# Performance work log

Measured on AMD Instinct MI355X. Metric: run time of the kernel, lower is better.

The kernel has to match this reference:

```python
import jax, jax.numpy as jnp
import numpy as np
from jax import lax

K = 8          # num_classes
C_IN = 256     # in_channels
EPS = 1e-5


def resize_bilinear_ac(x, H, W):
    """Bilinear resize with align_corners=True. x: [B,C,h,w] -> [B,C,H,W]."""
    B, C, h, w = x.shape
    if h == H and w == W:
        return x
    ys = jnp.linspace(0.0, h - 1.0, H)
    xs = jnp.linspace(0.0, w - 1.0, W)
    y0 = jnp.floor(ys).astype(jnp.int32)
    x0 = jnp.floor(xs).astype(jnp.int32)
    y1 = jnp.minimum(y0 + 1, h - 1)
    x1 = jnp.minimum(x0 + 1, w - 1)
    wy = (ys - y0.astype(x.dtype))[None, None, :, None]
    wx = (xs - x0.astype(x.dtype))[None, None, None, :]
    g00 = x[:, :, y0][:, :, :, x0]
    g01 = x[:, :, y0][:, :, :, x1]
    g10 = x[:, :, y1][:, :, :, x0]
    g11 = x[:, :, y1][:, :, :, x1]
    top = g00 * (1.0 - wx) + g01 * wx
    bot = g10 * (1.0 - wx) + g11 * wx
    return top * (1.0 - wy) + bot * wy


def setup_inputs() -> dict:
    key = jax.random.key(0)
    ks = jax.random.split(key, 16)
    shapes = [(2, 256, 128, 128), (2, 256, 64, 64), (2, 256, 32, 32), (2, 256, 16, 16), (2, 256, 8, 8)]
    inp = {}
    for i, s in enumerate(shapes):
        inp[f"feat{i}"] = jax.random.normal(ks[i], s, dtype=jnp.float32)
    inp["attr_feat"] = jax.random.normal(ks[5], (2, K * C_IN, 64, 64), dtype=jnp.float32)
    # learned params
    inp["mlp_f_w"] = jax.random.normal(ks[6], (256, 256), dtype=jnp.float32) * 0.02
    inp["mlp_f_b"] = jnp.zeros((256,), dtype=jnp.float32)
    inp["mlp_a_w"] = jax.random.normal(ks[7], (256, 256), dtype=jnp.float32) * 0.02
    inp["mlp_a_b"] = jnp.zeros((256,), dtype=jnp.float32)
    # 5 grouped convs: [out=2048, in_per_group=256, 3, 3] each, no bias (BN follows)
    inp["conv_w"] = jax.random.normal(ks[8], (5, K * C_IN, C_IN, 3, 3), dtype=jnp.float32) * 0.02
    inp["bn_gamma"] = jnp.ones((5, K * C_IN), dtype=jnp.float32)
    inp["bn_beta"] = jnp.zeros((5, K * C_IN), dtype=jnp.float32)
    inp["bn_mean"] = jax.random.normal(ks[9], (5, K * C_IN), dtype=jnp.float32) * 0.1
    inp["bn_var"] = jax.random.uniform(ks[10], (5, K * C_IN), dtype=jnp.float32, minval=0.5, maxval=1.5)
    return inp


def _forward(feats, attr_feat, mlp_f_w, mlp_f_b, mlp_a_w, mlp_a_b, conv_w, bn_gamma, bn_beta, bn_mean, bn_var):
    B = attr_feat.shape[0]
    # global avg pool attr -> [B, K, C] -> mlp_a
    avg_attr = attr_feat.mean(axis=(2, 3)).reshape(B, K, C_IN)
    avg_attr = avg_attr @ mlp_a_w.T + mlp_a_b  # [B,K,256]
    outs = []
    for i, x in enumerate(feats):
        _, C, H, W = x.shape
        avg_x = x.mean(axis=(2, 3)) @ mlp_f_w.T + mlp_f_b          # [B,256]
        logits = jnp.einsum('bkc,bc->bk', avg_attr, avg_x)          # [B,K]
        attn = jax.nn.softmax(logits, axis=-1)
        y = resize_bilinear_ac(attr_feat, H, W)                      # [B,2048,H,W]
        y = lax.conv_general_dilated(
            y, conv_w[i], window_strides=(1, 1), padding=((1, 1), (1, 1)),
            dimension_numbers=('NCHW', 'OIHW', 'NCHW'), feature_group_count=K)
        inv = lax.rsqrt(bn_var[i] + EPS)
        y = (y - bn_mean[i][None, :, None, None]) * (inv * bn_gamma[i])[None, :, None, None] + bn_beta[i][None, :, None, None]
        y = jax.nn.relu(y)
        y = y.reshape(B, K, C, H, W)
        y = jnp.einsum('bkchw,bk->bchw', y, attn)                   # weighted sum over classes
        outs.append(jax.nn.relu(x + y))
    return tuple(outs)


def reference(feat0, feat1, feat2, feat3, feat4, attr_feat, mlp_f_w, mlp_f_b, mlp_a_w, mlp_a_b, conv_w, bn_gamma, bn_beta, bn_mean, bn_var):
    feats = [feat0, feat1, feat2, feat3, feat4]
    return _forward(feats, attr_feat, mlp_f_w, mlp_f_b, mlp_a_w, mlp_a_b, conv_w, bn_gamma, bn_beta, bn_mean, bn_var)
```

## Files before the change

kernel.cpp:

```cpp
#include <hip/hip_runtime.h>
#include <hip/hip_bf16.h>
#include <cstdint>

typedef __attribute__((ext_vector_type(8))) short short8;
typedef __attribute__((ext_vector_type(4))) float f32x4;

#define EPSV 1e-5f

__device__ __forceinline__ void gload_lds16(const void* g, void* l) {
  __builtin_amdgcn_global_load_lds(
      (const __attribute__((address_space(1))) void*)(uintptr_t)g,
      (__attribute__((address_space(3))) void*)(uint32_t)(uintptr_t)l,
      16, 0, 0);
}

__global__ void mean_kernel(const float* __restrict__ in, float* __restrict__ out,
                            int HW, float inv) {
  const int ch = blockIdx.x;
  const int t = threadIdx.x;
  const float* p = in + (size_t)ch * HW;
  float s = 0.f;
  const int nv = HW >> 2;
  const float4* pv = (const float4*)p;
  for (int i = t; i < nv; i += 256) { float4 v = pv[i]; s += v.x + v.y + v.z + v.w; }
  __shared__ float red[256];
  red[t] = s; __syncthreads();
  for (int off = 128; off > 0; off >>= 1) {
    if (t < off) red[t] += red[t + off];
    __syncthreads();
  }
  if (t == 0) out[ch] = red[0] * inv;
}

__global__ void wtrans_kernel(const float* __restrict__ cw,
                              const float* __restrict__ gamma, const float* __restrict__ beta,
                              const float* __restrict__ mean, const float* __restrict__ var,
                              __hip_bfloat16* __restrict__ wt, float* __restrict__ bias) {
  const int oc = blockIdx.x;
  const int i  = blockIdx.y;
  const int ci = threadIdx.x;
  const int idx = i * 2048 + oc;
  const float sc = rsqrtf(var[idx] + EPSV) * gamma[idx];
  if (ci == 0) bias[idx] = beta[idx] - mean[idx] * sc;
  const int g = oc >> 8, co = oc & 255;
  const float* src = cw + ((size_t)idx * 256 + ci) * 9;
  const size_t dbase = (size_t)(i * 8 + g) * 9 * 65536 + co * 256 + ci;
#pragma unroll
  for (int tap = 0; tap < 9; ++tap)
    wt[dbase + (size_t)tap * 65536] = __float2bfloat16(src[tap] * sc);
}

__global__ void gate_kernel(const float* __restrict__ meanA, const float* __restrict__ meanF,
                            const float* __restrict__ Wa, const float* __restrict__ ba,
                            const float* __restrict__ Wf, const float* __restrict__ bfp,
                            float* __restrict__ attn) {
  __shared__ float mA[16 * 256];
  __shared__ float mF[10 * 256];
  __shared__ float pA[16 * 256];
  __shared__ float pF[10 * 256];
  __shared__ float lg[80];
  const int t = threadIdx.x;
  for (int i = t; i < 4096; i += 256) mA[i] = meanA[i];
  for (int i = t; i < 2560; i += 256) mF[i] = meanF[i];
  __syncthreads();
  {
    float acc[16];
#pragma unroll
    for (int j = 0; j < 16; ++j) acc[j] = 0.f;
    for (int ci = 0; ci < 256; ++ci) {
      const float w = Wa[t * 256 + ci];
#pragma unroll
      for (int j = 0; j < 16; ++j) acc[j] += mA[j * 256 + ci] * w;
    }
    const float bb = ba[t];
#pragma unroll
    for (int j = 0; j < 16; ++j) pA[j * 256 + t] = acc[j] + bb;
  }
  {
    float acc[10];
#pragma unroll
    for (int j = 0; j < 10; ++j) acc[j] = 0.f;
    for (int ci = 0; ci < 256; ++ci) {
      const float w = Wf[t * 256 + ci];
#pragma unroll
      for (int j = 0; j < 10; ++j) acc[j] += mF[j * 256 + ci] * w;
    }
    const float bb = bfp[t];
#pragma unroll
    for (int j = 0; j < 10; ++j) pF[j * 256 + t] = acc[j] + bb;
  }
  __syncthreads();
  if (t < 80) {
    const int i = t >> 4, r = t & 15, b = r >> 3, k = r & 7;
    const float* a = &pA[(b * 8 + k) * 256];
    const float* f = &pF[(i * 2 + b) * 256];
    float d = 0.f;
    for (int c = 0; c < 256; ++c) d += a[c] * f[c];
    lg[t] = d;
  }
  __syncthreads();
  if (t < 10) {
    const int base = t * 8;
    float m = lg[base];
    for (int k = 1; k < 8; ++k) m = fmaxf(m, lg[base + k]);
    float e[8], s = 0.f;
    for (int k = 0; k < 8; ++k) { e[k] = __expf(lg[base + k] - m); s += e[k]; }
    const float invs = 1.f / s;
    for (int k = 0; k < 8; ++k) attn[base + k] = e[k] * invs;
  }
}

__global__ void resize_kernel(const float* __restrict__ attr,
                              __hip_bfloat16* __restrict__ R,
                              int W, int Hp, int Wp, float scl) {
  const int bk = blockIdx.x;
  const int yp = blockIdx.y;
  const int t  = threadIdx.x;
  const size_t rowbase = ((size_t)bk * Hp + yp) * (size_t)Wp * 256;
  if (yp == 0 || yp == Hp - 1) {
    uint32_t* p = (uint32_t*)(R + rowbase);
    const int n = Wp * 128;
    for (int idx = t; idx < n; idx += 256) p[idx] = 0u;
    return;
  }
  const int y = yp - 1;
  const float fy = y * scl;
  int y0 = (int)floorf(fy); if (y0 > 63) y0 = 63;
  const float wy = fy - (float)y0;
  const int y1 = min(y0 + 1, 63);
  __shared__ float buf[2][64][65];
  const int cc = t >> 2, seg = (t & 3) * 16;
  const int bb = bk >> 3, k = bk & 7;
  const float* ab = attr + (size_t)bb * 2048 * 4096;
  const int ci = t & 63;
  for (int cq = 0; cq < 4; ++cq) {
    __syncthreads();
    {
      const int ch = k * 256 + cq * 64 + cc;
      const float* r0 = ab + ((size_t)ch * 64 + y0) * 64;
      const float* r1 = ab + ((size_t)ch * 64 + y1) * 64;
#pragma unroll
      for (int u = 0; u < 4; ++u) {
        float4 v0 = ((const float4*)r0)[(t & 3) * 4 + u];
        float4 v1 = ((const float4*)r1)[(t & 3) * 4 + u];
        buf[0][cc][seg + u * 4 + 0] = v0.x; buf[0][cc][seg + u * 4 + 1] = v0.y;
        buf[0][cc][seg + u * 4 + 2] = v0.z; buf[0][cc][seg + u * 4 + 3] = v0.w;
        buf[1][cc][seg + u * 4 + 0] = v1.x; buf[1][cc][seg + u * 4 + 1] = v1.y;
        buf[1][cc][seg + u * 4 + 2] = v1.z; buf[1][cc][seg + u * 4 + 3] = v1.w;
      }
    }
    __syncthreads();
    for (int x = t >> 6; x < W; x += 4) {
      const float fx = x * scl;
      int x0 = (int)floorf(fx); if (x0 > 63) x0 = 63;
      const float wx = fx - (float)x0;
      const int x1 = min(x0 + 1, 63);
      const float top = buf[0][ci][x0] * (1.f - wx) + buf[0][ci][x1] * wx;
      const float bot = buf[1][ci][x0] * (1.f - wx) + buf[1][ci][x1] * wx;
      R[rowbase + (size_t)(x + 1) * 256 + cq * 64 + ci] = __float2bfloat16(top * (1.f - wy) + bot * wy);
    }
    if (t < 64) {
      R[rowbase + cq * 64 + t] = __float2bfloat16(0.f);
      R[rowbase + (size_t)(Wp - 1) * 256 + cq * 64 + t] = __float2bfloat16(0.f);
    }
  }
}

__device__ __forceinline__ void issue_stage(
    const __hip_bfloat16* __restrict__ Wt, const __hip_bfloat16* __restrict__ Rb,
    size_t rgstride, int gp, int typ, int txp, int cqp, int Wp,
    const int* aoff, const int* adst, const int* boff, const int* bdst,
    __hip_bfloat16* bufA, __hip_bfloat16* bufB) {
  const __hip_bfloat16* wp = Wt + (((size_t)gp * 9 + typ * 3 + txp) << 16) + (cqp << 6);
  const __hip_bfloat16* rp = Rb + (size_t)gp * rgstride + ((typ * Wp + txp) << 8) + (cqp << 6);
#pragma unroll
  for (int q = 0; q < 4; ++q) gload_lds16(wp + aoff[q], bufA + adst[q]);
#pragma unroll
  for (int q = 0; q < 2; ++q) gload_lds16(rp + boff[q], bufB + bdst[q]);
}

__global__ __launch_bounds__(512, 2)
void conv_kernel(const __hip_bfloat16* __restrict__ R,
                 const __hip_bfloat16* __restrict__ Wt,
                 const float* __restrict__ bias,
                 const float* __restrict__ attn,
                 const float* __restrict__ featp,
                 float* __restrict__ outp,
                 int W, int lw, int Hp, int Wp, int HW,
                 int b0, int NB, int gcount) {
  __shared__ alignas(16) __hip_bfloat16 ldsA[3][256 * 64];
  __shared__ alignas(16) __hip_bfloat16 ldsB[3][128 * 64];
  const int tid  = threadIdx.x;
  const int lane = tid & 63;
  const int wave = __builtin_amdgcn_readfirstlane(tid >> 6);
  const int wm = (wave >> 1) * 64;
  const int wn = (wave & 1) * 64;
  const int n0  = blockIdx.x * 128;
  const int bb  = (int)blockIdx.y % NB;
  const int gs  = (int)blockIdx.y / NB;
  const int b   = b0 + bb;
  const int g0  = gs * gcount;

  const int c8 = lane & 7;
  const int r8 = lane >> 3;
  int aoff[4], adst[4], boff[2], bdst[2];
#pragma unroll
  for (int q = 0; q < 4; ++q) {
    const int row = wave * 32 + q * 8 + r8;
    aoff[q] = (row << 8) + ((c8 ^ (row & 7)) << 3);
    adst[q] = (wave * 32 + q * 8) << 6;
  }
#pragma unroll
  for (int q = 0; q < 2; ++q) {
    const int row = wave * 16 + q * 8 + r8;
    int sg = n0 + row; if (sg >= HW) sg = HW - 1;
    const int y = sg >> lw, x = sg & (W - 1);
    boff[q] = ((y * Wp + x) << 8) + ((c8 ^ (row & 7)) << 3);
    bdst[q] = (wave * 16 + q * 8) << 6;
  }

  const size_t rgstride = (size_t)Hp * Wp * 256;
  const __hip_bfloat16* Rb = R + (size_t)bb * 8 * rgstride;

  const f32x4 fz = {0.f, 0.f, 0.f, 0.f};
  f32x4 fin[4][4], acc[4][4];
#pragma unroll
  for (int mf = 0; mf < 4; ++mf)
#pragma unroll
    for (int nf = 0; nf < 4; ++nf) { fin[mf][nf] = fz; acc[mf][nf] = fz; }

  issue_stage(Wt, Rb, rgstride, g0, 0, 0, 0, Wp, aoff, adst, boff, bdst,
              &ldsA[0][0], &ldsB[0][0]);
  issue_stage(Wt, Rb, rgstride, g0, 0, 0, 1, Wp, aoff, adst, boff, bdst,
              &ldsA[1][0], &ldsB[1][0]);
  int cqp = 1, txp = 0, typ = 0, gp = g0;
  int cur = 0, nbf = 2;
  int foldc = 0, gcur = g0;
  const int nstages = gcount * 36;

  for (int s = 0; s < nstages; ++s) {
    __builtin_amdgcn_s_barrier();
    asm volatile("" ::: "memory");
    if (s + 2 < nstages) {
      ++cqp;
      if (cqp == 4) {
        cqp = 0; ++txp;
        if (txp == 3) { txp = 0; ++typ; if (typ == 3) { typ = 0; ++gp; } }
      }
      issue_stage(Wt, Rb, rgstride, gp, typ, txp, cqp, Wp, aoff, adst, boff, bdst,
                  &ldsA[nbf][0], &ldsB[nbf][0]);
      asm volatile("s_waitcnt vmcnt(12)" ::: "memory");
    } else if (s + 1 < nstages) {
      asm volatile("s_waitcnt vmcnt(6)" ::: "memory");
    } else {
      asm volatile("s_waitcnt vmcnt(0)" ::: "memory");
    }
    __builtin_amdgcn_s_barrier();
    asm volatile("" ::: "memory");

    const __hip_bfloat16* pA = &ldsA[cur][0];
    const __hip_bfloat16* pB = &ldsB[cur][0];
#pragma unroll
    for (int ks = 0; ks < 2; ++ks) {
      short8 af[4], bfv[4];
      const int cb = ks * 4 + (lane >> 4);
#pragma unroll
      for (int mf = 0; mf < 4; ++mf) {
        const int row = wm + mf * 16 + (lane & 15);
        af[mf] = *(const short8*)&pA[(row << 6) + ((cb ^ (row & 7)) << 3)];
      }
#pragma unroll
      for (int nf = 0; nf < 4; ++nf) {
        const int row = wn + nf * 16 + (lane & 15);
        bfv[nf] = *(const short8*)&pB[(row << 6) + ((cb ^ (row & 7)) << 3)];
      }
#pragma unroll
      for (int mf = 0; mf < 4; ++mf)
#pragma unroll
        for (int nf = 0; nf < 4; ++nf)
          acc[mf][nf] = __builtin_amdgcn_mfma_f32_16x16x32_bf16(
              af[mf], bfv[nf], acc[mf][nf], 0, 0, 0);
    }

    if (++cur == 3) cur = 0;
    if (++nbf == 3) nbf = 0;

    if (++foldc == 36) {
      foldc = 0;
      const float aw = attn[b * 8 + gcur];
#pragma unroll
      for (int mf = 0; mf < 4; ++mf) {
        const int cobase = wm + mf * 16 + ((lane >> 4) << 2);
#pragma unroll
        for (int r = 0; r < 4; ++r) {
          const float bs = bias[(gcur << 8) + cobase + r];
#pragma unroll
          for (int nf = 0; nf < 4; ++nf) {
            fin[mf][nf][r] += aw * fmaxf(acc[mf][nf][r] + bs, 0.f);
            acc[mf][nf][r] = 0.f;
          }
        }
      }
      ++gcur;
    }
  }

  const size_t plane = (size_t)256 * HW;
  if (featp) {
    const float* fb = featp + (size_t)b * plane;
    float* ob = outp + (size_t)b * plane;
#pragma unroll
    for (int mf = 0; mf < 4; ++mf) {
      const int cobase = wm + mf * 16 + ((lane >> 4) << 2);
#pragma unroll
      for (int nf = 0; nf < 4; ++nf) {
        const int n = n0 + wn + nf * 16 + (lane & 15);
        if (n < HW) {
#pragma unroll
          for (int r = 0; r < 4; ++r) {
            const size_t idx = (size_t)(cobase + r) * HW + n;
            ob[idx] = fmaxf(fb[idx] + fin[mf][nf][r], 0.f);
          }
        }
      }
    }
  } else {
    float* zb = outp + ((size_t)gs * 2 + b) * plane;
#pragma unroll
    for (int mf = 0; mf < 4; ++mf) {
      const int cobase = wm + mf * 16 + ((lane >> 4) << 2);
#pragma unroll
      for (int nf = 0; nf < 4; ++nf) {
        const int n = n0 + wn + nf * 16 + (lane & 15);
        if (n < HW) {
#pragma unroll
          for (int r = 0; r < 4; ++r)
            zb[(size_t)(cobase + r) * HW + n] = fin[mf][nf][r];
        }
      }
    }
  }
}

__global__ void reduce_kernel(const float* __restrict__ z, const float* __restrict__ feat,
                              float* __restrict__ outp, int total, int S) {
  const int idx = blockIdx.x * 256 + threadIdx.x;
  if (idx >= total) return;
  float s = feat[idx];
  for (int j = 0; j < S; ++j) s += z[(size_t)j * total + idx];
  outp[idx] = fmaxf(s, 0.f);
}

extern "C" void kernel_launch(void* const* d_in, const int* in_sizes, int n_in,
                              void* d_out, int out_size, void* d_ws, size_t ws_size,
                              hipStream_t stream) {
  const float* feat[5];
  for (int i = 0; i < 5; ++i) feat[i] = (const float*)d_in[i];
  const float* attr = (const float*)d_in[5];
  const float* mfw = (const float*)d_in[6];
  const float* mfb = (const float*)d_in[7];
  const float* maw = (const float*)d_in[8];
  const float* mab = (const float*)d_in[9];
  const float* cw  = (const float*)d_in[10];
  const float* bng = (const float*)d_in[11];
  const float* bnb = (const float*)d_in[12];
  const float* bnm = (const float*)d_in[13];
  const float* bnv = (const float*)d_in[14];
  float* out = (float*)d_out;

  char* ws = (char*)d_ws;
  float* attnW = (float*)(ws);
  float* meanA = (float*)(ws + 512);
  float* meanF = (float*)(ws + 20480);
  float* biasW = (float*)(ws + 32768);
  __hip_bfloat16* Wt = (__hip_bfloat16*)(ws + 131072);
  const size_t R_OFF = 47316992;
  __hip_bfloat16* Rbuf = (__hip_bfloat16*)(ws + R_OFF);

  const bool full = ws_size >= (size_t)219316224;
  const int NB = full ? 2 : 1;
  float* zbuf = (float*)(ws + R_OFF + (size_t)NB * 69222400);

  static const int HS[5] = {128, 64, 32, 16, 8};
  static const size_t OOFF[5] = {0, 8388608, 10485760, 11010048, 11141120};
  static const int SPLIT[5] = {1, 4, 8, 8, 8};

  mean_kernel<<<4096, 256, 0, stream>>>(attr, meanA, 4096, 1.f / 4096.f);
  for (int i = 0; i < 5; ++i) {
    const int HW = HS[i] * HS[i];
    mean_kernel<<<512, 256, 0, stream>>>(feat[i], meanF + i * 512, HW, 1.f / (float)HW);
  }
  wtrans_kernel<<<dim3(2048, 5), 256, 0, stream>>>(cw, bng, bnb, bnm, bnv, Wt, biasW);
  gate_kernel<<<1, 256, 0, stream>>>(meanA, meanF, maw, mab, mfw, mfb, attnW);

  for (int i = 0; i < 5; ++i) {
    const int H = HS[i], W = H, HW = H * W, Hp = H + 2, Wp = W + 2;
    const int lw = 31 - __builtin_clz((unsigned)W);
    const float scl = 63.f / (float)(H - 1);
    const int S = full ? SPLIT[i] : 1;
    const int gcount = 8 / S;
    for (int b0 = 0; b0 < 2; b0 += NB) {
      resize_kernel<<<dim3(NB * 8, Hp), 256, 0, stream>>>(
          attr + (size_t)b0 * 2048 * 4096, Rbuf, W, Hp, Wp, scl);
      const float* fp = (S == 1) ? feat[i] : nullptr;
      float* op = (S == 1) ? (out + OOFF[i]) : zbuf;
      conv_kernel<<<dim3((HW + 127) / 128, NB * S), 512, 0, stream>>>(
          Rbuf, Wt + (size_t)i * 8 * 9 * 65536, biasW + i * 2048, attnW + i * 16,
          fp, op, W, lw, Hp, Wp, HW, b0, NB, gcount);
    }
    if (S > 1) {
      const int total = 2 * 256 * HW;
      reduce_kernel<<<(total + 255) / 256, 256, 0, stream>>>(zbuf, feat[i], out + OOFF[i], total, S);
    }
  }
}
```

Baseline: 822.7 us.

## Split main loop into ping-pong LDS-read/MFMA phases with barriers and setprio

Restructures the GEMM main loop so each stage is two half-K phases. Each phase reads fragments from LDS, issues the next global-to-LDS prefetch, then runs its MFMA cluster at raised wave priority between barriers. The vmcnt waits are moved and the prologue now waits before the loop starts. The aim is to interleave waves so LDS reads and global loads overlap other waves' MFMA work. The cost is more barriers per stage and a tighter, easy-to-get-wrong wait/hazard ordering across the triple-buffered LDS.

```diff
diff --git a/kernel.cpp b/kernel.cpp
--- a/kernel.cpp
+++ b/kernel.cpp
@@ -233,14 +233,33 @@
               &ldsA[0][0], &ldsB[0][0]);
   issue_stage(Wt, Rb, rgstride, g0, 0, 0, 1, Wp, aoff, adst, boff, bdst,
               &ldsA[1][0], &ldsB[1][0]);
+  asm volatile("s_waitcnt vmcnt(6)" ::: "memory");
+  __builtin_amdgcn_s_barrier();
+  asm volatile("" ::: "memory");
+
   int cqp = 1, txp = 0, typ = 0, gp = g0;
   int cur = 0, nbf = 2;
   int foldc = 0, gcur = g0;
   const int nstages = gcount * 36;
 
   for (int s = 0; s < nstages; ++s) {
-    __builtin_amdgcn_s_barrier();
-    asm volatile("" ::: "memory");
+    const __hip_bfloat16* pA = &ldsA[cur][0];
+    const __hip_bfloat16* pB = &ldsB[cur][0];
+    short8 af[4], bfv[4];
+
+    {
+      const int cb = lane >> 4;
+#pragma unroll
+      for (int mf = 0; mf < 4; ++mf) {
+        const int row = wm + mf * 16 + (lane & 15);
+        af[mf] = *(const short8*)&pA[(row << 6) + ((cb ^ (row & 7)) << 3)];
+      }
+#pragma unroll
+      for (int nf = 0; nf < 4; ++nf) {
+        const int row = wn + nf * 16 + (lane & 15);
+        bfv[nf] = *(const short8*)&pB[(row << 6) + ((cb ^ (row & 7)) << 3)];
+      }
+    }
     if (s + 2 < nstages) {
       ++cqp;
       if (cqp == 4) {
@@ -249,21 +268,22 @@
       }
       issue_stage(Wt, Rb, rgstride, gp, typ, txp, cqp, Wp, aoff, adst, boff, bdst,
                   &ldsA[nbf][0], &ldsB[nbf][0]);
-      asm volatile("s_waitcnt vmcnt(12)" ::: "memory");
-    } else if (s + 1 < nstages) {
-      asm volatile("s_waitcnt vmcnt(6)" ::: "memory");
-    } else {
-      asm volatile("s_waitcnt vmcnt(0)" ::: "memory");
-    }
+    }
+    __builtin_amdgcn_s_barrier();
+    __builtin_amdgcn_sched_barrier(0);
+    __builtin_amdgcn_s_setprio(1);
+#pragma unroll
+    for (int mf = 0; mf < 4; ++mf)
+#pragma unroll
+      for (int nf = 0; nf < 4; ++nf)
+        acc[mf][nf] = __builtin_amdgcn_mfma_f32_16x16x32_bf16(
+            af[mf], bfv[nf], acc[mf][nf], 0, 0, 0);
+    __builtin_amdgcn_s_setprio(0);
     __builtin_amdgcn_s_barrier();
     asm volatile("" ::: "memory");
 
-    const __hip_bfloat16* pA = &ldsA[cur][0];
-    const __hip_bfloat16* pB = &ldsB[cur][0];
-#pragma unroll
-    for (int ks = 0; ks < 2; ++ks) {
-      short8 af[4], bfv[4];
-      const int cb = ks * 4 + (lane >> 4);
+    {
+      const int cb = 4 + (lane >> 4);
 #pragma unroll
       for (int mf = 0; mf < 4; ++mf) {
         const int row = wm + mf * 16 + (lane & 15);
@@ -274,13 +294,21 @@
         const int row = wn + nf * 16 + (lane & 15);
         bfv[nf] = *(const short8*)&pB[(row << 6) + ((cb ^ (row & 7)) << 3)];
       }
-#pragma unroll
-      for (int mf = 0; mf < 4; ++mf)
-#pragma unroll
-        for (int nf = 0; nf < 4; ++nf)
-          acc[mf][nf] = __builtin_amdgcn_mfma_f32_16x16x32_bf16(
-              af[mf], bfv[nf], acc[mf][nf], 0, 0, 0);
-    }
+    }
+    if (s + 2 < nstages)      asm volatile("s_waitcnt vmcnt(6)" ::: "memory");
+    else if (s + 1 < nstages) asm volatile("s_waitcnt vmcnt(0)" ::: "memory");
+    __builtin_amdgcn_s_barrier();
+    __builtin_amdgcn_sched_barrier(0);
+    __builtin_amdgcn_s_setprio(1);
+#pragma unroll
+    for (int mf = 0; mf < 4; ++mf)
+#pragma unroll
+      for (int nf = 0; nf < 4; ++nf)
+        acc[mf][nf] = __builtin_amdgcn_mfma_f32_16x16x32_bf16(
+            af[mf], bfv[nf], acc[mf][nf], 0, 0, 0);
+    __builtin_amdgcn_s_setprio(0);
+    __builtin_amdgcn_s_barrier();
+    asm volatile("" ::: "memory");
 
     if (++cur == 3) cur = 0;
     if (++nbf == 3) nbf = 0;
```

Result: no change. 822.8 us (+0.0%).
